# Performance work log

Measured on AMD Instinct MI355X. Metric: run time of the kernel, lower is better.

The kernel has to match this reference:

```python
import jax, jax.numpy as jnp
import numpy as np

NUM_LAYERS = 2
HIDDEN = 256
BATCH = 64
SEQ = 2048


def setup_inputs() -> dict:
    key = jax.random.key(0)
    ks = jax.random.split(key, 8)
    H, L = HIDDEN, NUM_LAYERS
    s = 1.0 / np.sqrt(H)  # PyTorch LSTM init scale (uniform(-s, s)); use normal*s for simplicity
    inp = {
        "input": jax.random.normal(ks[0], (BATCH, SEQ, H), dtype=jnp.float32),
        # stacked per-layer weights; input size == hidden size so shapes are uniform
        "w_ih": jax.random.normal(ks[1], (L, 4 * H, H), dtype=jnp.float32) * s,
        "w_hh": jax.random.normal(ks[2], (L, 4 * H, H), dtype=jnp.float32) * s,
        "b_ih": jax.random.normal(ks[3], (L, 4 * H), dtype=jnp.float32) * s,
        "b_hh": jax.random.normal(ks[4], (L, 4 * H), dtype=jnp.float32) * s,
        "w_lin": jax.random.normal(ks[5], (1, H), dtype=jnp.float32) * s,
        "b_lin": jax.random.normal(ks[6], (1,), dtype=jnp.float32) * s,
    }
    return inp


def _lstm_layer(x, w_ih, w_hh, b_ih, b_hh):
    """One LSTM layer over x: [B, T, H] -> outputs [B, T, H], final (h, c).
    PyTorch gate order: i, f, g, o."""
    B, T, H = x.shape
    # precompute input contribution to gates for all timesteps: [T, B, 4H]
    xg = (jnp.einsum('bth,gh->btg', x, w_ih) + b_ih).transpose(1, 0, 2)

    def step(carry, xg_t):
        h, c = carry
        gates = xg_t + h @ w_hh.T + b_hh  # [B, 4H]
        i, f, g, o = jnp.split(gates, 4, axis=-1)
        i = jax.nn.sigmoid(i)
        f = jax.nn.sigmoid(f)
        g = jnp.tanh(g)
        o = jax.nn.sigmoid(o)
        c = f * c + i * g
        h = o * jnp.tanh(c)
        return (h, c), h

    h0 = jnp.zeros((B, H), dtype=x.dtype)
    c0 = jnp.zeros((B, H), dtype=x.dtype)
    (h, c), ys = jax.lax.scan(step, (h0, c0), xg)
    return ys.transpose(1, 0, 2), (h, c)


def reference(input, w_ih, w_hh, b_ih, b_hh, w_lin, b_lin):
    x = input
    for l in range(NUM_LAYERS):
        x, (h, c) = _lstm_layer(x, w_ih[l], w_hh[l], b_ih[l], b_hh[l])
    # output[:, -1, :] == final hidden state of top layer (all lengths == T)
    last = x[:, -1, :]
    out = last @ w_lin.T + b_lin  # [B, 1]
    return out
```

## Files before the change

### kernel.cpp

```cpp
#include <hip/hip_runtime.h>
#include <math.h>

#define HID   256
#define GATES 1024
#define BATCH 64
#define SEQ   2048

#define BM 128
#define BN 128
#define BK 16
#define LDP 132

__global__ __launch_bounds__(256, 2)
void xg_gemm(const float* __restrict__ A, const float* __restrict__ W,
             const float* __restrict__ bias, float* __restrict__ out,
             int a_bstride, int ch_log2)
{
    __shared__ float As[BK][LDP];
    __shared__ float Ws[BK][LDP];

    const int tid   = threadIdx.x;
    const int m_blk = blockIdx.x * BM;
    const int n_blk = blockIdx.y * BN;

    const int tn = (tid & 15) * 4;
    const int tm = (tid >> 4) * 4;

    float acc[8][8];
    #pragma unroll
    for (int i = 0; i < 8; ++i)
        #pragma unroll
        for (int j = 0; j < 8; ++j) acc[i][j] = 0.f;

    const int lrow = tid >> 2;
    const int lkc  = (tid & 3) * 4;
    const int CHm1 = (1 << ch_log2) - 1;

    for (int k0 = 0; k0 < HID; k0 += BK) {
        #pragma unroll
        for (int p = 0; p < 2; ++p) {
            int row = p * 64 + lrow;
            int r   = m_blk + row;
            int b   = r >> ch_log2;
            int t   = r & CHm1;
            const float4 a = *(const float4*)(A + (size_t)b * a_bstride +
                                              (size_t)t * HID + k0 + lkc);
            As[lkc + 0][row] = a.x;
            As[lkc + 1][row] = a.y;
            As[lkc + 2][row] = a.z;
            As[lkc + 3][row] = a.w;

            int g = n_blk + row;
            const float4 w = *(const float4*)(W + (size_t)g * HID + k0 + lkc);
            Ws[lkc + 0][row] = w.x;
            Ws[lkc + 1][row] = w.y;
            Ws[lkc + 2][row] = w.z;
            Ws[lkc + 3][row] = w.w;
        }
        __syncthreads();

        #pragma unroll
        for (int kk = 0; kk < BK; ++kk) {
            float4 a0 = *(const float4*)&As[kk][tm];
            float4 a1 = *(const float4*)&As[kk][tm + 64];
            float4 b0 = *(const float4*)&Ws[kk][tn];
            float4 b1 = *(const float4*)&Ws[kk][tn + 64];
            float av[8] = {a0.x, a0.y, a0.z, a0.w, a1.x, a1.y, a1.z, a1.w};
            float bv[8] = {b0.x, b0.y, b0.z, b0.w, b1.x, b1.y, b1.z, b1.w};
            #pragma unroll
            for (int i = 0; i < 8; ++i)
                #pragma unroll
                for (int j = 0; j < 8; ++j)
                    acc[i][j] += av[i] * bv[j];
        }
        __syncthreads();
    }

    const float4 bias0 = *(const float4*)&bias[n_blk + tn];
    const float4 bias1 = *(const float4*)&bias[n_blk + tn + 64];
    #pragma unroll
    for (int i = 0; i < 8; ++i) {
        int m  = (i < 4) ? (tm + i) : (tm + 60 + i);
        int gm = m_blk + m;
        float* op = out + (size_t)gm * GATES + n_blk;
        float4 v0 = {acc[i][0] + bias0.x, acc[i][1] + bias0.y,
                     acc[i][2] + bias0.z, acc[i][3] + bias0.w};
        float4 v1 = {acc[i][4] + bias1.x, acc[i][5] + bias1.y,
                     acc[i][6] + bias1.z, acc[i][7] + bias1.w};
        *(float4*)(op + tn)      = v0;
        *(float4*)(op + tn + 64) = v1;
    }
}

#define MBSTRIDE ((size_t)BATCH * HID)

__device__ __forceinline__ float sigmoid_f(float x) {
    return 1.f / (1.f + __expf(-x));
}
__device__ __forceinline__ float tanh_f(float x) {
    return 1.f - 2.f / (1.f + __expf(2.f * x));
}

__global__ __launch_bounds__(1024, 4)
void lstm_rec_v10(const float* __restrict__ xg1, const float* __restrict__ xg2,
                  const float* __restrict__ w_hh, const float* __restrict__ b_hh,
                  unsigned long long* mb1, unsigned long long* mb2,
                  float* __restrict__ cs1, float* __restrict__ cs2,
                  float* __restrict__ h1ch,
                  int CH, int gbaseA, int gbaseB, int doA, int doB)
{
    __shared__ __attribute__((aligned(16))) float hsh[2][16 * 20];
    __shared__ __attribute__((aligned(16))) float part[2][16][260];
    __shared__ float occ_pad[11264];

    const int bid   = blockIdx.x;
    const int layer = bid >> 7;
    if (layer == 0 && !doA) return;
    if (layer == 1 && !doB) return;
    if (CH < 0) occ_pad[threadIdx.x] = 1.f;

    const int lid = bid & 127;
    const int s   = lid & 3;
    const int b0  = (lid >> 2) * 2;
    const int tid = threadIdx.x;
    const int kc  = tid & 15;
    const int u   = tid >> 4;
    const int gu  = s * 64 + u;

    const float* xgL = layer ? xg2 : xg1;
    const float* wL  = w_hh + (size_t)layer * GATES * HID;
    const float* bL  = b_hh + layer * GATES;
    unsigned long long* mbL = layer ? mb2 : mb1;
    float* csL = layer ? cs2 : cs1;
    const int gbase = layer ? gbaseB : gbaseA;

    float4 wreg[4][4];
    #pragma unroll
    for (int j = 0; j < 4; ++j) {
        const float* wr = wL + (size_t)(j * 256 + gu) * HID + kc * 16;
        #pragma unroll
        for (int i = 0; i < 4; ++i) {
            float4 w = *(const float4*)(wr + 4 * i);
            asm volatile("" : "+v"(w.x), "+v"(w.y), "+v"(w.z), "+v"(w.w));
            wreg[j][i] = w;
        }
    }

    const int bq_o = tid >> 6;
    const int u_o  = tid & 63;
    const int gu_o = s * 64 + u_o;
    float c_u = 0.f;
    float bh[4] = {0.f, 0.f, 0.f, 0.f};
    if (tid < 128) {
        c_u = csL[(b0 + bq_o) * HID + gu_o];
        #pragma unroll
        for (int g = 0; g < 4; ++g) bh[g] = bL[g * 256 + gu_o];
    }

    const int bq_p  = tid >> 8;
    const int hid_p = tid & 255;

    for (int t = 0; t < CH; ++t) {
        const int gt = gbase + t;
        const int pr = gt & 1;

        float xv[4];
        if (tid < 128) {
            const float* xp = xgL + ((size_t)(b0 + bq_o) * CH + t) * GATES;
            #pragma unroll
            for (int g = 0; g < 4; ++g) xv[g] = xp[g * 256 + gu_o];
        }

        if (tid < 512) {
            const unsigned long long* slot =
                mbL + (size_t)pr * MBSTRIDE + (b0 + bq_p) * HID + hid_p;
            unsigned long long w;
            do {
                w = __hip_atomic_load(slot, __ATOMIC_RELAXED,
                                      __HIP_MEMORY_SCOPE_AGENT);
            } while ((unsigned)(w >> 32) != (unsigned)gt);
            hsh[bq_p][(hid_p >> 4) * 20 + (hid_p & 15)] =
                __uint_as_float((unsigned)w);
        }
        __syncthreads();

        #pragma unroll
        for (int bq = 0; bq < 2; ++bq) {
            const float4* hq = (const float4*)&hsh[bq][kc * 20];
            float4 h0 = hq[0], h1 = hq[1], h2 = hq[2], h3 = hq[3];
            float4 pv;
            float* pp = (float*)&pv;
            #pragma unroll
            for (int j = 0; j < 4; ++j) {
                float a = wreg[j][0].x * h0.x + wreg[j][0].y * h0.y
                        + wreg[j][0].z * h0.z + wreg[j][0].w * h0.w;
                a += wreg[j][1].x * h1.x + wreg[j][1].y * h1.y
                   + wreg[j][1].z * h1.z + wreg[j][1].w * h1.w;
                a += wreg[j][2].x * h2.x + wreg[j][2].y * h2.y
                   + wreg[j][2].z * h2.z + wreg[j][2].w * h2.w;
                a += wreg[j][3].x * h3.x + wreg[j][3].y * h3.y
                   + wreg[j][3].z * h3.z + wreg[j][3].w * h3.w;
                pp[j] = a;
            }
            *(float4*)&part[bq][kc][4 * u] = pv;
        }
        __syncthreads();

        if (tid < 128) {
            float gx = 0.f, gy = 0.f, gz = 0.f, gw = 0.f;
            #pragma unroll
            for (int k = 0; k < 16; ++k) {
                float4 pk = *(const float4*)&part[bq_o][k][4 * u_o];
                gx += pk.x; gy += pk.y; gz += pk.z; gw += pk.w;
            }
            float ig = sigmoid_f(gx + xv[0] + bh[0]);
            float fg = sigmoid_f(gy + xv[1] + bh[1]);
            float gv = tanh_f   (gz + xv[2] + bh[2]);
            float og = sigmoid_f(gw + xv[3] + bh[3]);
            c_u = fg * c_u + ig * gv;
            float h = og * tanh_f(c_u);

            __hip_atomic_store(
                mbL + (size_t)((gt + 1) & 1) * MBSTRIDE + (b0 + bq_o) * HID + gu_o,
                ((unsigned long long)(unsigned)(gt + 1) << 32) |
                    (unsigned long long)__float_as_uint(h),
                __ATOMIC_RELAXED, __HIP_MEMORY_SCOPE_AGENT);

            if (layer == 0)
                h1ch[((size_t)(b0 + bq_o) * CH + t) * HID + gu_o] = h;
        }
    }

    if (tid < 128) csL[(b0 + bq_o) * HID + gu_o] = c_u;
}

__global__ void final_linear(const unsigned long long* __restrict__ hw,
                             const float* __restrict__ w_lin,
                             const float* __restrict__ b_lin,
                             float* __restrict__ out)
{
    int b = blockIdx.x;
    int l = threadIdx.x;
    float p = 0.f;
    #pragma unroll
    for (int j = 0; j < 4; ++j) {
        int u = l + j * 64;
        p += __uint_as_float((unsigned)hw[b * HID + u]) * w_lin[u];
    }
    #pragma unroll
    for (int off = 32; off > 0; off >>= 1) p += __shfl_down(p, off, 64);
    if (l == 0) out[b] = p + b_lin[0];
}

extern "C" void kernel_launch(void* const* d_in, const int* in_sizes, int n_in,
                              void* d_out, int out_size, void* d_ws, size_t ws_size,
                              hipStream_t stream)
{
    const float* input = (const float*)d_in[0];
    const float* w_ih  = (const float*)d_in[1];
    const float* w_hh  = (const float*)d_in[2];
    const float* b_ih  = (const float*)d_in[3];
    const float* b_hh  = (const float*)d_in[4];
    const float* w_lin = (const float*)d_in[5];
    const float* b_lin = (const float*)d_in[6];
    float* out = (float*)d_out;

    const size_t c_elems  = (size_t)BATCH * HID;
    const size_t mb_bytes = 2 * MBSTRIDE * sizeof(unsigned long long);
    char*  ws   = (char*)d_ws;
    float* cs1  = (float*)ws;
    float* cs2  = cs1 + c_elems;
    unsigned long long* mb1 = (unsigned long long*)(cs2 + c_elems);
    unsigned long long* mb2 = mb1 + 2 * MBSTRIDE;
    const size_t zero_bytes = 2 * c_elems * 4 + 2 * mb_bytes;
    float* big  = (float*)(ws + ((zero_bytes + 255) & ~(size_t)255));

    int CH = 256;
    while (CH > 16) {
        size_t need = ((zero_bytes + 255) & ~(size_t)255)
                    + ((size_t)2 * BATCH * CH * GATES + (size_t)BATCH * CH * HID) * 4;
        if (need <= ws_size) break;
        CH >>= 1;
    }
    const int ch_log2 = __builtin_ctz((unsigned)CH);

    float* xg1  = big;
    float* xg2  = xg1 + (size_t)BATCH * CH * GATES;
    float* h1ch = xg2 + (size_t)BATCH * CH * GATES;

    hipMemsetAsync(ws, 0, zero_bytes, stream);

    const int NC = SEQ / CH;
    dim3 gblk(BATCH * CH / BM, GATES / BN);

    for (int c = 0; c <= NC; ++c) {
        if (c < NC)
            xg_gemm<<<gblk, 256, 0, stream>>>(input + (size_t)c * CH * HID, w_ih,
                                              b_ih, xg1, SEQ * HID, ch_log2);
        if (c >= 1)
            xg_gemm<<<gblk, 256, 0, stream>>>(h1ch, w_ih + (size_t)GATES * HID,
                                              b_ih + GATES, xg2, CH * HID, ch_log2);
        lstm_rec_v10<<<256, 1024, 0, stream>>>(xg1, xg2, w_hh, b_hh, mb1, mb2,
                                               cs1, cs2, h1ch, CH,
                                               c * CH, (c - 1) * CH,
                                               (c < NC) ? 1 : 0, (c >= 1) ? 1 : 0);
    }

    final_linear<<<BATCH, 64, 0, stream>>>(mb2, w_lin, b_lin, out);
}
```

Measured before the change: 7.041 ms.

## Software-pipeline the two batch rows in the LSTM recurrence step

Each timestep is split into two half-phases, one per batch row. The matvec for one row now overlaps with the polling and gate/cell update of the other row, and the second row's epilogue is deferred into the next iteration. This is meant to hide cross-block spin-wait latency and activation math behind useful FMA work. Polling moves to the upper 256 threads, and the occupancy padding in shared memory shrinks. In exchange the loop has four barriers per step instead of two, plus a tail epilogue, and the xv and cell-state handling per row becomes more intricate.

Measured after the change: 6.092 ms, median of 2. 1.16x faster.

```diff
diff --git a/kernel.cpp b/kernel.cpp
--- a/kernel.cpp
+++ b/kernel.cpp
@@ -102,7 +102,7 @@
 }
 
 __global__ __launch_bounds__(1024, 4)
-void lstm_rec_v10(const float* __restrict__ xg1, const float* __restrict__ xg2,
+void lstm_rec_v11(const float* __restrict__ xg1, const float* __restrict__ xg2,
                   const float* __restrict__ w_hh, const float* __restrict__ b_hh,
                   unsigned long long* mb1, unsigned long long* mb2,
                   float* __restrict__ cs1, float* __restrict__ cs2,
@@ -111,13 +111,18 @@
 {
     __shared__ __attribute__((aligned(16))) float hsh[2][16 * 20];
     __shared__ __attribute__((aligned(16))) float part[2][16][260];
-    __shared__ float occ_pad[11264];
+    __shared__ float occ_pad[3328];
 
     const int bid   = blockIdx.x;
     const int layer = bid >> 7;
     if (layer == 0 && !doA) return;
     if (layer == 1 && !doB) return;
-    if (CH < 0) occ_pad[threadIdx.x] = 1.f;
+
+    if (gbaseA == 0x7fffffff) {
+        volatile float* vp = occ_pad;
+        vp[threadIdx.x] = (float)CH;
+        cs1[0] = vp[threadIdx.x ^ 1];
+    }
 
     const int lid = bid & 127;
     const int s   = lid & 3;
@@ -146,47 +151,63 @@
         }
     }
 
-    const int bq_o = tid >> 6;
     const int u_o  = tid & 63;
     const int gu_o = s * 64 + u_o;
+    const int b_o  = b0 + ((tid >> 6) & 1);
     float c_u = 0.f;
     float bh[4] = {0.f, 0.f, 0.f, 0.f};
+    float xv[4] = {0.f, 0.f, 0.f, 0.f};
     if (tid < 128) {
-        c_u = csL[(b0 + bq_o) * HID + gu_o];
+        c_u = csL[b_o * HID + gu_o];
         #pragma unroll
         for (int g = 0; g < 4; ++g) bh[g] = bL[g * 256 + gu_o];
     }
 
-    const int bq_p  = tid >> 8;
-    const int hid_p = tid & 255;
+    const int pt = tid - 768;
 
     for (int t = 0; t < CH; ++t) {
         const int gt = gbase + t;
         const int pr = gt & 1;
 
-        float xv[4];
-        if (tid < 128) {
-            const float* xp = xgL + ((size_t)(b0 + bq_o) * CH + t) * GATES;
-            #pragma unroll
-            for (int g = 0; g < 4; ++g) xv[g] = xp[g * 256 + gu_o];
-        }
-
-        if (tid < 512) {
+        if (tid >= 768) {
             const unsigned long long* slot =
-                mbL + (size_t)pr * MBSTRIDE + (b0 + bq_p) * HID + hid_p;
+                mbL + (size_t)pr * MBSTRIDE + b0 * HID + pt;
             unsigned long long w;
             do {
                 w = __hip_atomic_load(slot, __ATOMIC_RELAXED,
                                       __HIP_MEMORY_SCOPE_AGENT);
             } while ((unsigned)(w >> 32) != (unsigned)gt);
-            hsh[bq_p][(hid_p >> 4) * 20 + (hid_p & 15)] =
-                __uint_as_float((unsigned)w);
-        }
-        __syncthreads();
-
-        #pragma unroll
-        for (int bq = 0; bq < 2; ++bq) {
-            const float4* hq = (const float4*)&hsh[bq][kc * 20];
+            hsh[0][(pt >> 4) * 20 + (pt & 15)] = __uint_as_float((unsigned)w);
+        } else if (tid < 128) {
+            if ((tid & 64) && t > 0) {
+                float gx = 0.f, gy = 0.f, gz = 0.f, gw = 0.f;
+                #pragma unroll
+                for (int k = 0; k < 16; ++k) {
+                    float4 pk = *(const float4*)&part[1][k][4 * u_o];
+                    gx += pk.x; gy += pk.y; gz += pk.z; gw += pk.w;
+                }
+                float ig = sigmoid_f(gx + xv[0] + bh[0]);
+                float fg = sigmoid_f(gy + xv[1] + bh[1]);
+                float gv = tanh_f   (gz + xv[2] + bh[2]);
+                float og = sigmoid_f(gw + xv[3] + bh[3]);
+                c_u = fg * c_u + ig * gv;
+                float h = og * tanh_f(c_u);
+                __hip_atomic_store(
+                    mbL + (size_t)(gt & 1) * MBSTRIDE + b_o * HID + gu_o,
+                    ((unsigned long long)(unsigned)gt << 32) |
+                        (unsigned long long)__float_as_uint(h),
+                    __ATOMIC_RELAXED, __HIP_MEMORY_SCOPE_AGENT);
+                if (layer == 0)
+                    h1ch[((size_t)b_o * CH + (t - 1)) * HID + gu_o] = h;
+            }
+            const float* xp = xgL + ((size_t)b_o * CH + t) * GATES;
+            #pragma unroll
+            for (int g = 0; g < 4; ++g) xv[g] = xp[g * 256 + gu_o];
+        }
+        __syncthreads();
+
+        {
+            const float4* hq = (const float4*)&hsh[0][kc * 20];
             float4 h0 = hq[0], h1 = hq[1], h2 = hq[2], h3 = hq[3];
             float4 pv;
             float* pp = (float*)&pv;
@@ -202,15 +223,15 @@
                    + wreg[j][3].z * h3.z + wreg[j][3].w * h3.w;
                 pp[j] = a;
             }
-            *(float4*)&part[bq][kc][4 * u] = pv;
-        }
-        __syncthreads();
-
-        if (tid < 128) {
+            *(float4*)&part[0][kc][4 * u] = pv;
+        }
+        __syncthreads();
+
+        if (tid < 64) {
             float gx = 0.f, gy = 0.f, gz = 0.f, gw = 0.f;
             #pragma unroll
             for (int k = 0; k < 16; ++k) {
-                float4 pk = *(const float4*)&part[bq_o][k][4 * u_o];
+                float4 pk = *(const float4*)&part[0][k][4 * u_o];
                 gx += pk.x; gy += pk.y; gz += pk.z; gw += pk.w;
             }
             float ig = sigmoid_f(gx + xv[0] + bh[0]);
@@ -219,19 +240,71 @@
             float og = sigmoid_f(gw + xv[3] + bh[3]);
             c_u = fg * c_u + ig * gv;
             float h = og * tanh_f(c_u);
-
             __hip_atomic_store(
-                mbL + (size_t)((gt + 1) & 1) * MBSTRIDE + (b0 + bq_o) * HID + gu_o,
+                mbL + (size_t)((gt + 1) & 1) * MBSTRIDE + b_o * HID + gu_o,
                 ((unsigned long long)(unsigned)(gt + 1) << 32) |
                     (unsigned long long)__float_as_uint(h),
                 __ATOMIC_RELAXED, __HIP_MEMORY_SCOPE_AGENT);
-
             if (layer == 0)
-                h1ch[((size_t)(b0 + bq_o) * CH + t) * HID + gu_o] = h;
-        }
-    }
-
-    if (tid < 128) csL[(b0 + bq_o) * HID + gu_o] = c_u;
+                h1ch[((size_t)b_o * CH + t) * HID + gu_o] = h;
+        } else if (tid >= 768) {
+            const unsigned long long* slot =
+                mbL + (size_t)pr * MBSTRIDE + (b0 + 1) * HID + pt;
+            unsigned long long w;
+            do {
+                w = __hip_atomic_load(slot, __ATOMIC_RELAXED,
+                                      __HIP_MEMORY_SCOPE_AGENT);
+            } while ((unsigned)(w >> 32) != (unsigned)gt);
+            hsh[1][(pt >> 4) * 20 + (pt & 15)] = __uint_as_float((unsigned)w);
+        }
+        __syncthreads();
+
+        {
+            const float4* hq = (const float4*)&hsh[1][kc * 20];
+            float4 h0 = hq[0], h1 = hq[1], h2 = hq[2], h3 = hq[3];
+            float4 pv;
+            float* pp = (float*)&pv;
+            #pragma unroll
+            for (int j = 0; j < 4; ++j) {
+                float a = wreg[j][0].x * h0.x + wreg[j][0].y * h0.y
+                        + wreg[j][0].z * h0.z + wreg[j][0].w * h0.w;
+                a += wreg[j][1].x * h1.x + wreg[j][1].y * h1.y
+                   + wreg[j][1].z * h1.z + wreg[j][1].w * h1.w;
+                a += wreg[j][2].x * h2.x + wreg[j][2].y * h2.y
+                   + wreg[j][2].z * h2.z + wreg[j][2].w * h2.w;
+                a += wreg[j][3].x * h3.x + wreg[j][3].y * h3.y
+                   + wreg[j][3].z * h3.z + wreg[j][3].w * h3.w;
+                pp[j] = a;
+            }
+            *(float4*)&part[1][kc][4 * u] = pv;
+        }
+        __syncthreads();
+    }
+
+    if (tid >= 64 && tid < 128) {
+        const int gt_e = gbase + CH;
+        float gx = 0.f, gy = 0.f, gz = 0.f, gw = 0.f;
+        #pragma unroll
+        for (int k = 0; k < 16; ++k) {
+            float4 pk = *(const float4*)&part[1][k][4 * u_o];
+            gx += pk.x; gy += pk.y; gz += pk.z; gw += pk.w;
+        }
+        float ig = sigmoid_f(gx + xv[0] + bh[0]);
+        float fg = sigmoid_f(gy + xv[1] + bh[1]);
+        float gv = tanh_f   (gz + xv[2] + bh[2]);
+        float og = sigmoid_f(gw + xv[3] + bh[3]);
+        c_u = fg * c_u + ig * gv;
+        float h = og * tanh_f(c_u);
+        __hip_atomic_store(
+            mbL + (size_t)(gt_e & 1) * MBSTRIDE + b_o * HID + gu_o,
+            ((unsigned long long)(unsigned)gt_e << 32) |
+                (unsigned long long)__float_as_uint(h),
+            __ATOMIC_RELAXED, __HIP_MEMORY_SCOPE_AGENT);
+        if (layer == 0)
+            h1ch[((size_t)b_o * CH + (CH - 1)) * HID + gu_o] = h;
+    }
+
+    if (tid < 128) csL[b_o * HID + gu_o] = c_u;
 }
 
 __global__ void final_linear(const unsigned long long* __restrict__ hw,
@@ -300,7 +373,7 @@
         if (c >= 1)
             xg_gemm<<<gblk, 256, 0, stream>>>(h1ch, w_ih + (size_t)GATES * HID,
                                               b_ih + GATES, xg2, CH * HID, ch_log2);
-        lstm_rec_v10<<<256, 1024, 0, stream>>>(xg1, xg2, w_hh, b_hh, mb1, mb2,
+        lstm_rec_v11<<<256, 1024, 0, stream>>>(xg1, xg2, w_hh, b_hh, mb1, mb2,
                                                cs1, cs2, h1ch, CH,
                                                c * CH, (c - 1) * CH,
                                                (c < NC) ? 1 : 0, (c >= 1) ? 1 : 0);
```

## Reduce gate partials with shuffles, pipeline two batch rows, remap blocks per XCD

Applied to the files above, without the earlier changes.

Replaces the shared-memory partial-sum buffer and second barrier with 16-lane shuffle reductions, so the kc==0 lanes compute the gates directly. The two batch rows are now processed one after another within each timestep, so row 1 can be polled while row 0's update is already published. Blocks are remapped so that each batch group's four slice blocks share an XCD, and the occupancy padding array is dropped. This aims to cut barrier and LDS overhead on the latency-bound recurrence. The cost is that each row needs its own barrier-separated phase, and only 1 in 16 threads does the nonlinear update.

New measurement: 7.811 ms. 1.11x slower.

```diff
diff --git a/kernel.cpp b/kernel.cpp
--- a/kernel.cpp
+++ b/kernel.cpp
@@ -102,7 +102,7 @@
 }
 
 __global__ __launch_bounds__(1024, 4)
-void lstm_rec_v10(const float* __restrict__ xg1, const float* __restrict__ xg2,
+void lstm_rec_v12(const float* __restrict__ xg1, const float* __restrict__ xg2,
                   const float* __restrict__ w_hh, const float* __restrict__ b_hh,
                   unsigned long long* mb1, unsigned long long* mb2,
                   float* __restrict__ cs1, float* __restrict__ cs2,
@@ -110,18 +110,17 @@
                   int CH, int gbaseA, int gbaseB, int doA, int doB)
 {
     __shared__ __attribute__((aligned(16))) float hsh[2][16 * 20];
-    __shared__ __attribute__((aligned(16))) float part[2][16][260];
-    __shared__ float occ_pad[11264];
-
-    const int bid   = blockIdx.x;
-    const int layer = bid >> 7;
+
+    const int bid = blockIdx.x;
+    const int xcd   = bid & 7;
+    const int mm    = bid >> 3;
+    const int s     = mm & 3;
+    const int G     = (mm >> 2) * 8 + xcd;
+    const int layer = G >> 5;
+    const int b0    = (G & 31) * 2;
     if (layer == 0 && !doA) return;
     if (layer == 1 && !doB) return;
-    if (CH < 0) occ_pad[threadIdx.x] = 1.f;
-
-    const int lid = bid & 127;
-    const int s   = lid & 3;
-    const int b0  = (lid >> 2) * 2;
+
     const int tid = threadIdx.x;
     const int kc  = tid & 15;
     const int u   = tid >> 4;
@@ -146,47 +145,43 @@
         }
     }
 
-    const int bq_o = tid >> 6;
-    const int u_o  = tid & 63;
-    const int gu_o = s * 64 + u_o;
-    float c_u = 0.f;
+    const bool upd = (kc == 0);
+    float c0 = 0.f, c1 = 0.f;
     float bh[4] = {0.f, 0.f, 0.f, 0.f};
-    if (tid < 128) {
-        c_u = csL[(b0 + bq_o) * HID + gu_o];
-        #pragma unroll
-        for (int g = 0; g < 4; ++g) bh[g] = bL[g * 256 + gu_o];
-    }
-
-    const int bq_p  = tid >> 8;
-    const int hid_p = tid & 255;
+    if (upd) {
+        c0 = csL[b0 * HID + gu];
+        c1 = csL[(b0 + 1) * HID + gu];
+        #pragma unroll
+        for (int g = 0; g < 4; ++g) bh[g] = bL[g * 256 + gu];
+    }
 
     for (int t = 0; t < CH; ++t) {
         const int gt = gbase + t;
         const int pr = gt & 1;
 
-        float xv[4];
-        if (tid < 128) {
-            const float* xp = xgL + ((size_t)(b0 + bq_o) * CH + t) * GATES;
-            #pragma unroll
-            for (int g = 0; g < 4; ++g) xv[g] = xp[g * 256 + gu_o];
-        }
-
-        if (tid < 512) {
+        float xv0[4], xv1[4];
+        if (upd) {
+            const float* xp0 = xgL + ((size_t)b0 * CH + t) * GATES;
+            const float* xp1 = xgL + ((size_t)(b0 + 1) * CH + t) * GATES;
+            #pragma unroll
+            for (int g = 0; g < 4; ++g) xv0[g] = xp0[g * 256 + gu];
+            #pragma unroll
+            for (int g = 0; g < 4; ++g) xv1[g] = xp1[g * 256 + gu];
+        }
+        if (tid < 256) {
             const unsigned long long* slot =
-                mbL + (size_t)pr * MBSTRIDE + (b0 + bq_p) * HID + hid_p;
+                mbL + (size_t)pr * MBSTRIDE + b0 * HID + tid;
             unsigned long long w;
             do {
                 w = __hip_atomic_load(slot, __ATOMIC_RELAXED,
                                       __HIP_MEMORY_SCOPE_AGENT);
             } while ((unsigned)(w >> 32) != (unsigned)gt);
-            hsh[bq_p][(hid_p >> 4) * 20 + (hid_p & 15)] =
-                __uint_as_float((unsigned)w);
+            hsh[0][(tid >> 4) * 20 + (tid & 15)] = __uint_as_float((unsigned)w);
         }
         __syncthreads();
 
-        #pragma unroll
-        for (int bq = 0; bq < 2; ++bq) {
-            const float4* hq = (const float4*)&hsh[bq][kc * 20];
+        {
+            const float4* hq = (const float4*)&hsh[0][kc * 20];
             float4 h0 = hq[0], h1 = hq[1], h2 = hq[2], h3 = hq[3];
             float4 pv;
             float* pp = (float*)&pv;
@@ -202,36 +197,88 @@
                    + wreg[j][3].z * h3.z + wreg[j][3].w * h3.w;
                 pp[j] = a;
             }
-            *(float4*)&part[bq][kc][4 * u] = pv;
+            #pragma unroll
+            for (int off = 8; off > 0; off >>= 1) {
+                pv.x += __shfl_down(pv.x, off, 16);
+                pv.y += __shfl_down(pv.y, off, 16);
+                pv.z += __shfl_down(pv.z, off, 16);
+                pv.w += __shfl_down(pv.w, off, 16);
+            }
+            if (upd) {
+                float ig = sigmoid_f(pv.x + xv0[0] + bh[0]);
+                float fg = sigmoid_f(pv.y + xv0[1] + bh[1]);
+                float gv = tanh_f   (pv.z + xv0[2] + bh[2]);
+                float og = sigmoid_f(pv.w + xv0[3] + bh[3]);
+                c0 = fg * c0 + ig * gv;
+                float h = og * tanh_f(c0);
+                __hip_atomic_store(
+                    mbL + (size_t)((gt + 1) & 1) * MBSTRIDE + b0 * HID + gu,
+                    ((unsigned long long)(unsigned)(gt + 1) << 32) |
+                        (unsigned long long)__float_as_uint(h),
+                    __ATOMIC_RELAXED, __HIP_MEMORY_SCOPE_AGENT);
+                if (layer == 0)
+                    h1ch[((size_t)b0 * CH + t) * HID + gu] = h;
+            }
+        }
+
+        if (tid < 256) {
+            const unsigned long long* slot =
+                mbL + (size_t)pr * MBSTRIDE + (b0 + 1) * HID + tid;
+            unsigned long long w;
+            do {
+                w = __hip_atomic_load(slot, __ATOMIC_RELAXED,
+                                      __HIP_MEMORY_SCOPE_AGENT);
+            } while ((unsigned)(w >> 32) != (unsigned)gt);
+            hsh[1][(tid >> 4) * 20 + (tid & 15)] = __uint_as_float((unsigned)w);
         }
         __syncthreads();
 
-        if (tid < 128) {
-            float gx = 0.f, gy = 0.f, gz = 0.f, gw = 0.f;
-            #pragma unroll
-            for (int k = 0; k < 16; ++k) {
-                float4 pk = *(const float4*)&part[bq_o][k][4 * u_o];
-                gx += pk.x; gy += pk.y; gz += pk.z; gw += pk.w;
-            }
-            float ig = sigmoid_f(gx + xv[0] + bh[0]);
-            float fg = sigmoid_f(gy + xv[1] + bh[1]);
-            float gv = tanh_f   (gz + xv[2] + bh[2]);
-            float og = sigmoid_f(gw + xv[3] + bh[3]);
-            c_u = fg * c_u + ig * gv;
-            float h = og * tanh_f(c_u);
-
-            __hip_atomic_store(
-                mbL + (size_t)((gt + 1) & 1) * MBSTRIDE + (b0 + bq_o) * HID + gu_o,
-                ((unsigned long long)(unsigned)(gt + 1) << 32) |
-                    (unsigned long long)__float_as_uint(h),
-                __ATOMIC_RELAXED, __HIP_MEMORY_SCOPE_AGENT);
-
-            if (layer == 0)
-                h1ch[((size_t)(b0 + bq_o) * CH + t) * HID + gu_o] = h;
-        }
-    }
-
-    if (tid < 128) csL[(b0 + bq_o) * HID + gu_o] = c_u;
+        {
+            const float4* hq = (const float4*)&hsh[1][kc * 20];
+            float4 h0 = hq[0], h1 = hq[1], h2 = hq[2], h3 = hq[3];
+            float4 pv;
+            float* pp = (float*)&pv;
+            #pragma unroll
+            for (int j = 0; j < 4; ++j) {
+                float a = wreg[j][0].x * h0.x + wreg[j][0].y * h0.y
+                        + wreg[j][0].z * h0.z + wreg[j][0].w * h0.w;
+                a += wreg[j][1].x * h1.x + wreg[j][1].y * h1.y
+                   + wreg[j][1].z * h1.z + wreg[j][1].w * h1.w;
+                a += wreg[j][2].x * h2.x + wreg[j][2].y * h2.y
+                   + wreg[j][2].z * h2.z + wreg[j][2].w * h2.w;
+                a += wreg[j][3].x * h3.x + wreg[j][3].y * h3.y
+                   + wreg[j][3].z * h3.z + wreg[j][3].w * h3.w;
+                pp[j] = a;
+            }
+            #pragma unroll
+            for (int off = 8; off > 0; off >>= 1) {
+                pv.x += __shfl_down(pv.x, off, 16);
+                pv.y += __shfl_down(pv.y, off, 16);
+                pv.z += __shfl_down(pv.z, off, 16);
+                pv.w += __shfl_down(pv.w, off, 16);
+            }
+            if (upd) {
+                float ig = sigmoid_f(pv.x + xv1[0] + bh[0]);
+                float fg = sigmoid_f(pv.y + xv1[1] + bh[1]);
+                float gv = tanh_f   (pv.z + xv1[2] + bh[2]);
+                float og = sigmoid_f(pv.w + xv1[3] + bh[3]);
+                c1 = fg * c1 + ig * gv;
+                float h = og * tanh_f(c1);
+                __hip_atomic_store(
+                    mbL + (size_t)((gt + 1) & 1) * MBSTRIDE + (b0 + 1) * HID + gu,
+                    ((unsigned long long)(unsigned)(gt + 1) << 32) |
+                        (unsigned long long)__float_as_uint(h),
+                    __ATOMIC_RELAXED, __HIP_MEMORY_SCOPE_AGENT);
+                if (layer == 0)
+                    h1ch[((size_t)(b0 + 1) * CH + t) * HID + gu] = h;
+            }
+        }
+    }
+
+    if (upd) {
+        csL[b0 * HID + gu]       = c0;
+        csL[(b0 + 1) * HID + gu] = c1;
+    }
 }
 
 __global__ void final_linear(const unsigned long long* __restrict__ hw,
@@ -300,7 +347,7 @@
         if (c >= 1)
             xg_gemm<<<gblk, 256, 0, stream>>>(h1ch, w_ih + (size_t)GATES * HID,
                                               b_ih + GATES, xg2, CH * HID, ch_log2);
-        lstm_rec_v10<<<256, 1024, 0, stream>>>(xg1, xg2, w_hh, b_hh, mb1, mb2,
+        lstm_rec_v12<<<256, 1024, 0, stream>>>(xg1, xg2, w_hh, b_hh, mb1, mb2,
                                                cs1, cs2, h1ch, CH,
                                                c * CH, (c - 1) * CH,
                                                (c < NC) ? 1 : 0, (c >= 1) ? 1 : 0);
```
